# Kernel optimization log

Measured on AMD Instinct MI355X. Metric: run time of the kernel, lower is better.

Reference implementation:

```python
import jax, jax.numpy as jnp
import numpy as np

B, L, E, DK = 16, 2048, 1024, 128
MODE = "Decoder"


def setup_inputs() -> dict:
    key = jax.random.key(0)
    ks = jax.random.split(key, 6)
    x = jax.random.normal(ks[0], (B, L, E), dtype=jnp.float32)
    context = jax.random.normal(ks[1], (B, L, E), dtype=jnp.float32)
    batch_lengths = jax.random.randint(ks[2], (B,), 1, L + 1)  # valid lengths in [1, L]
    Wq = jax.random.normal(ks[3], (E, DK), dtype=jnp.float32) * 0.02
    Wk = jax.random.normal(ks[4], (E, DK), dtype=jnp.float32) * 0.02
    Wv = jax.random.normal(ks[5], (E, DK), dtype=jnp.float32) * 0.02
    return {"x": x, "context": context, "batch_lengths": batch_lengths,
            "Wq": Wq, "Wk": Wk, "Wv": Wv, "max_len": L}


def reference(x, context, batch_lengths, Wq, Wk, Wv, max_len):
    # x, context: [B, L, E]; batch_lengths: [B] ints; weights: [E, DK]
    Lq = x.shape[1]
    dk = Wq.shape[1]
    pos = jnp.arange(Lq)
    # outputMask: zero out padded time steps, broadcast over feature dim [B, L, 1]
    len_mask = (pos[None, :] < batch_lengths[:, None]).astype(x.dtype)[:, :, None]
    Q = (context @ Wq) * len_mask
    K = (context @ Wk) * len_mask
    V = (x @ Wv) * len_mask
    # energy: [B, Lq, Lk]
    energy = jnp.einsum("bqd,bkd->bqk", Q, K)
    # attnMask: -inf on padded key positions
    key_valid = pos[None, None, :] < batch_lengths[:, None, None]  # [B,1,Lk]
    if MODE == "Decoder":
        causal = pos[None, :, None] >= pos[None, None, :]  # j <= i
        key_valid = key_valid & causal
    energy = jnp.where(key_valid, energy, -jnp.inf)
    score = jax.nn.softmax(energy / jnp.sqrt(jnp.asarray(dk, x.dtype)), axis=-1)
    return jnp.einsum("bqk,bkd->bqd", score, V)
```

## Files before the change

kernel.cpp:

```cpp
#include <hip/hip_runtime.h>

#define DEV __device__ __forceinline__

typedef __attribute__((ext_vector_type(4))) float f32x4;
typedef __attribute__((ext_vector_type(4))) unsigned short u16x4;
typedef __attribute__((ext_vector_type(8))) __bf16 bf16x8;

constexpr int NB = 16, SL = 2048, EM = 1024, DKD = 128;

DEV unsigned short f2bf(float f) {
  unsigned int u = __float_as_uint(f);
  u += 0x7FFFu + ((u >> 16) & 1u);
  return (unsigned short)(u >> 16);
}

DEV f32x4 mfma16(bf16x8 a, bf16x8 b, f32x4 c) {
  return __builtin_amdgcn_mfma_f32_16x16x32_bf16(a, b, c, 0, 0, 0);
}

DEV void dma16(const void* g, void* l) {
  __builtin_amdgcn_global_load_lds(
      (const __attribute__((address_space(1))) unsigned int*)g,
      (__attribute__((address_space(3))) unsigned int*)l, 16, 0, 0);
}

DEV bf16x8 cvt8(f32x4 a, f32x4 b) {
  bf16x8 r;
  r[0] = (__bf16)a[0]; r[1] = (__bf16)a[1]; r[2] = (__bf16)a[2]; r[3] = (__bf16)a[3];
  r[4] = (__bf16)b[0]; r[5] = (__bf16)b[1]; r[6] = (__bf16)b[2]; r[7] = (__bf16)b[3];
  return r;
}

#define SBAR() __builtin_amdgcn_sched_barrier(0)

__global__ __launch_bounds__(256) void prep_w(
    const float* __restrict__ Wq, const float* __restrict__ Wk,
    const float* __restrict__ Wv, unsigned short* __restrict__ Wt)
{
  __shared__ unsigned short T[64 * 128];
  const int tid = threadIdx.x;
  const int m = blockIdx.x >> 4, kc = blockIdx.x & 15;
  const float* W = (m == 0) ? Wq : ((m == 1) ? Wk : Wv);
  #pragma unroll
  for (int it = 0; it < 8; ++it) {
    int idx = it * 256 + tid;
    int kk = idx >> 5, n4 = (idx & 31) * 4;
    f32x4 w4 = *(const f32x4*)(W + (size_t)(kc * 64 + kk) * DKD + n4);
    *(u16x4*)&T[kk * 128 + n4] =
        u16x4{ f2bf(w4[0]), f2bf(w4[1]), f2bf(w4[2]), f2bf(w4[3]) };
  }
  __syncthreads();
  #pragma unroll
  for (int it = 0; it < 4; ++it) {
    int idx = it * 256 + tid;
    int p = idx & 7, n = idx >> 3;
    int c = p ^ (n & 7);
    unsigned short v[8];
    #pragma unroll
    for (int e = 0; e < 8; ++e) v[e] = T[(c * 8 + e) * 128 + n];
    size_t t = ((size_t)(m * 16 + kc) * 128 + n) * 8 + p;
    *(u16x4*)(Wt + t * 8)     = u16x4{v[0], v[1], v[2], v[3]};
    *(u16x4*)(Wt + t * 8 + 4) = u16x4{v[4], v[5], v[6], v[7]};
  }
}

__global__ __launch_bounds__(256, 2) void proj_qk(
    const float* __restrict__ ctx, const unsigned short* __restrict__ Wt,
    const int* __restrict__ lens, unsigned short* __restrict__ Qo,
    unsigned short* __restrict__ Kz)
{
  __shared__ float Als[2][64 * 64];
  const int tid = threadIdx.x;
  const int wave = tid >> 6, lane = tid & 63;
  const int quad = lane >> 4, mm = lane & 15;
  const int rb = blockIdx.x * 64;
  const int len = lens[blockIdx.x >> 5];
  if ((rb & (SL - 1)) >= len) return;

  f32x4 acc[4][4];
  #pragma unroll
  for (int i = 0; i < 4; ++i)
    #pragma unroll
    for (int j = 0; j < 4; ++j) acc[i][j] = f32x4{0.f, 0.f, 0.f, 0.f};

  const float* asrc[4];
  #pragma unroll
  for (int i = 0; i < 4; ++i) {
    const int rl_ = wave * 16 + i * 4 + (lane >> 4);
    const int cc  = (lane & 8) | ((lane & 7) ^ (rl_ & 7));
    asrc[i] = ctx + (size_t)(rb + rl_) * EM + cc * 4;
  }
  int soff[2][2];
  #pragma unroll
  for (int ks = 0; ks < 2; ++ks) {
    soff[ks][0] = (ks * 8 + ((quad * 2)     ^ (mm & 7))) * 4;
    soff[ks][1] = (ks * 8 + ((quad * 2 + 1) ^ (mm & 7))) * 4;
  }
  const unsigned short* bbase[4][2];
  #pragma unroll
  for (int lo = 0; lo < 4; ++lo)
    #pragma unroll
    for (int ks = 0; ks < 2; ++ks) {
      const int nrow = (wave * 4 + lo) * 16 + mm;
      const int pp = (ks * 4 + quad) ^ (mm & 7);
      const int cs = nrow * 8 + pp;
      bbase[lo][ks] = Wt + ((size_t)(cs >> 10) * 16384 + (cs & 1023)) * 8;
    }

  #pragma unroll
  for (int i = 0; i < 4; ++i)
    dma16(asrc[i],      (char*)Als[0] + wave * 4096 + i * 1024);
  #pragma unroll
  for (int i = 0; i < 4; ++i)
    dma16(asrc[i] + 64, (char*)Als[1] + wave * 4096 + i * 1024);
  __asm__ volatile("s_waitcnt vmcnt(4)" ::: "memory");
  __builtin_amdgcn_s_barrier();

  #pragma unroll 1
  for (int kc = 0; kc < 16; ++kc) {
    SBAR();
    bf16x8 bfr[4][2];
    #pragma unroll
    for (int lo = 0; lo < 4; ++lo)
      #pragma unroll
      for (int ks = 0; ks < 2; ++ks)
        bfr[lo][ks] = *(const bf16x8*)(bbase[lo][ks] + (size_t)kc * 8192);
    bf16x8 af[4][2];
    #pragma unroll
    for (int rt = 0; rt < 4; ++rt) {
      const float* rbase = Als[kc & 1] + (rt * 16 + mm) * 64;
      #pragma unroll
      for (int ks = 0; ks < 2; ++ks) {
        f32x4 a0 = *(const f32x4*)(rbase + soff[ks][0]);
        f32x4 a1 = *(const f32x4*)(rbase + soff[ks][1]);
        af[rt][ks] = cvt8(a0, a1);
      }
    }
    __asm__ volatile("s_waitcnt lgkmcnt(0)" ::: "memory");
    SBAR();
    __builtin_amdgcn_s_barrier();
    {
      const int kn = (kc + 2 < 16) ? (kc + 2) : 15;
      #pragma unroll
      for (int i = 0; i < 4; ++i)
        dma16(asrc[i] + kn * 64, (char*)Als[kc & 1] + wave * 4096 + i * 1024);
    }
    #pragma unroll
    for (int lo = 0; lo < 4; ++lo)
      #pragma unroll
      for (int ks = 0; ks < 2; ++ks)
        #pragma unroll
        for (int rt = 0; rt < 4; ++rt)
          acc[rt][lo] = mfma16(af[rt][ks], bfr[lo][ks], acc[rt][lo]);
    __builtin_amdgcn_s_barrier();
  }
  __asm__ volatile("s_waitcnt vmcnt(0)" ::: "memory");

  const float SCALE = 1.4426950408889634f * 0.08838834764831845f;
  #pragma unroll
  for (int rt = 0; rt < 4; ++rt)
    #pragma unroll
    for (int lo = 0; lo < 4; ++lo) {
      const int ctg = wave * 4 + lo;
      #pragma unroll
      for (int reg = 0; reg < 4; ++reg) {
        const int row = rb + rt * 16 + quad * 4 + reg;
        const int j = row & (SL - 1);
        const float val = acc[rt][lo][reg];
        if (ctg < 8) {
          const int d = ctg * 16 + mm;
          Qo[(size_t)row * DKD + d] = f2bf(val * ((j < len) ? SCALE : 0.f));
        } else {
          const int d = (ctg - 8) * 16 + mm;
          Kz[(size_t)row * DKD + (((d >> 3) ^ (j & 15)) * 8) + (d & 7)] = f2bf(val);
        }
      }
    }
}

__global__ __launch_bounds__(256, 2) void proj_v(
    const float* __restrict__ x, const unsigned short* __restrict__ Wt,
    const int* __restrict__ lens, unsigned short* __restrict__ Vz)
{
  __shared__ float Als[2][64 * 64];
  const int tid = threadIdx.x;
  const int wave = tid >> 6, lane = tid & 63;
  const int quad = lane >> 4, mm = lane & 15;
  const int rb = blockIdx.x * 64;
  const int len = lens[blockIdx.x >> 5];
  if ((rb & (SL - 1)) >= len) return;

  f32x4 acc[4][2];
  #pragma unroll
  for (int i = 0; i < 4; ++i) { acc[i][0] = f32x4{0.f,0.f,0.f,0.f}; acc[i][1] = f32x4{0.f,0.f,0.f,0.f}; }

  const float* asrc[4];
  #pragma unroll
  for (int i = 0; i < 4; ++i) {
    const int rl_ = wave * 16 + i * 4 + (lane >> 4);
    const int cc  = (lane & 8) | ((lane & 7) ^ (rl_ & 7));
    asrc[i] = x + (size_t)(rb + rl_) * EM + cc * 4;
  }
  int soff[2][2];
  #pragma unroll
  for (int ks = 0; ks < 2; ++ks) {
    soff[ks][0] = (ks * 8 + ((quad * 2)     ^ (mm & 7))) * 4;
    soff[ks][1] = (ks * 8 + ((quad * 2 + 1) ^ (mm & 7))) * 4;
  }
  const unsigned short* bbase[2][2];
  #pragma unroll
  for (int lo = 0; lo < 2; ++lo)
    #pragma unroll
    for (int ks = 0; ks < 2; ++ks) {
      const int nrow = (wave * 2 + lo) * 16 + mm;
      const int pp = (ks * 4 + quad) ^ (mm & 7);
      const int cs = nrow * 8 + pp;
      bbase[lo][ks] = Wt + ((size_t)2 * 16384 + cs) * 8;
    }

  #pragma unroll
  for (int i = 0; i < 4; ++i)
    dma16(asrc[i],      (char*)Als[0] + wave * 4096 + i * 1024);
  #pragma unroll
  for (int i = 0; i < 4; ++i)
    dma16(asrc[i] + 64, (char*)Als[1] + wave * 4096 + i * 1024);
  __asm__ volatile("s_waitcnt vmcnt(4)" ::: "memory");
  __builtin_amdgcn_s_barrier();

  #pragma unroll 1
  for (int kc = 0; kc < 16; ++kc) {
    SBAR();
    bf16x8 bfr[2][2];
    #pragma unroll
    for (int lo = 0; lo < 2; ++lo)
      #pragma unroll
      for (int ks = 0; ks < 2; ++ks)
        bfr[lo][ks] = *(const bf16x8*)(bbase[lo][ks] + (size_t)kc * 8192);
    bf16x8 af[4][2];
    #pragma unroll
    for (int rt = 0; rt < 4; ++rt) {
      const float* rbase = Als[kc & 1] + (rt * 16 + mm) * 64;
      #pragma unroll
      for (int ks = 0; ks < 2; ++ks) {
        f32x4 a0 = *(const f32x4*)(rbase + soff[ks][0]);
        f32x4 a1 = *(const f32x4*)(rbase + soff[ks][1]);
        af[rt][ks] = cvt8(a0, a1);
      }
    }
    __asm__ volatile("s_waitcnt lgkmcnt(0)" ::: "memory");
    SBAR();
    __builtin_amdgcn_s_barrier();
    {
      const int kn = (kc + 2 < 16) ? (kc + 2) : 15;
      #pragma unroll
      for (int i = 0; i < 4; ++i)
        dma16(asrc[i] + kn * 64, (char*)Als[kc & 1] + wave * 4096 + i * 1024);
    }
    #pragma unroll
    for (int lo = 0; lo < 2; ++lo)
      #pragma unroll
      for (int ks = 0; ks < 2; ++ks)
        #pragma unroll
        for (int rt = 0; rt < 4; ++rt)
          acc[rt][lo] = mfma16(af[rt][ks], bfr[lo][ks], acc[rt][lo]);
    __builtin_amdgcn_s_barrier();
  }
  __asm__ volatile("s_waitcnt vmcnt(0)" ::: "memory");

  #pragma unroll
  for (int rt = 0; rt < 4; ++rt)
    #pragma unroll
    for (int lo = 0; lo < 2; ++lo) {
      const int d = (wave * 2 + lo) * 16 + mm;
      const int row0 = rb + rt * 16 + quad * 4;
      const int b = row0 >> 11, j0 = row0 & (SL - 1);
      u16x4 pk = u16x4{ f2bf(acc[rt][lo][0]), f2bf(acc[rt][lo][1]),
                        f2bf(acc[rt][lo][2]), f2bf(acc[rt][lo][3]) };
      size_t off = (size_t)b * DKD * SL + (size_t)d * SL + (j0 & ~63)
                 + ((((j0 >> 3) & 7) ^ (d & 7)) * 8) + (j0 & 7);
      *(u16x4*)(Vz + off) = pk;
    }
}

__global__ __launch_bounds__(256, 2) void attn(
    const unsigned short* __restrict__ Qw, const unsigned short* __restrict__ Kz,
    const unsigned short* __restrict__ Vz, const int* __restrict__ lens,
    float* __restrict__ out)
{
  __shared__ unsigned short Ks[2][64 * 128];
  __shared__ unsigned short Vs[2][128 * 64];
  __shared__ unsigned short Ps[4][16 * 72];
  __shared__ float mv[128];
  const int tid = threadIdx.x;
  const int wave = tid >> 6, lane = tid & 63;
  const int quad = lane >> 4, mm = lane & 15;
  const int b = blockIdx.y;
  const int qb = ((int)gridDim.x - 1 - (int)blockIdx.x) * 64;
  const int len = lens[b];

  if (qb >= len) {
    const int half = tid >> 7, d = tid & 127, d7 = d & 7;
    const unsigned short* vbase = Vz + (size_t)b * DKD * SL + (size_t)d * SL;
    float sum = 0.f;
    for (int j0 = half * 64; j0 < len; j0 += 128) {
      #pragma unroll
      for (int cc = 0; cc < 8; ++cc) {
        const int jstart = j0 + cc * 8;
        if (jstart >= len) break;
        const unsigned short* p = vbase + j0 + ((cc ^ d7) * 8);
        if (jstart + 8 <= len) {
          bf16x8 v = *(const bf16x8*)p;
          sum += (float)v[0] + (float)v[1] + (float)v[2] + (float)v[3]
               + (float)v[4] + (float)v[5] + (float)v[6] + (float)v[7];
        } else {
          for (int r = 0; r < 8; ++r)
            if (jstart + r < len) sum += (float)*(const __bf16*)(p + r);
        }
      }
    }
    if (half == 0) mv[d] = sum;
    __syncthreads();
    if (half == 1) mv[d] += sum;
    __syncthreads();
    const float val = mv[d] / (float)len;
    #pragma unroll 1
    for (int it = 0; it < 32; ++it) {
      const int row = qb + half + it * 2;
      out[((size_t)b * SL + row) * DKD + d] = val;
    }
    return;
  }

  const int kend = min(qb + 64, len);
  const int nblk = (kend + 63) >> 6;
  const int irow0 = qb + wave * 16 + quad * 4;

  bf16x8 aQ[4];
  {
    const unsigned short* qbase =
        Qw + (size_t)(b * SL + qb + wave * 16 + mm) * DKD + quad * 8;
    #pragma unroll
    for (int cc = 0; cc < 4; ++cc) aQ[cc] = *(const bf16x8*)(qbase + cc * 32);
  }
  float mr[4], lr[4];
  #pragma unroll
  for (int r = 0; r < 4; ++r) { mr[r] = -__builtin_inff(); lr[r] = 0.f; }
  f32x4 acc[8];
  #pragma unroll
  for (int i = 0; i < 8; ++i) acc[i] = f32x4{0.f,0.f,0.f,0.f};

  #pragma unroll
  for (int it = 0; it < 4; ++it) {
    int s = it * 256 + tid;
    dma16(Kz + (size_t)(b * SL) * DKD + (size_t)s * 8,
          (char*)Ks[0] + (it * 256 + wave * 64) * 16);
  }
  #pragma unroll
  for (int it = 0; it < 4; ++it) {
    int s = it * 256 + tid;
    int d = s >> 3, p = s & 7;
    dma16(Vz + (size_t)b * DKD * SL + (size_t)d * SL + p * 8,
          (char*)Vs[0] + (it * 256 + wave * 64) * 16);
  }

  #pragma unroll 1
  for (int blk = 0; blk < nblk; ++blk) {
    const int kb = blk * 64;
    __syncthreads();
    if (blk + 1 < nblk) {
      const int kb1 = kb + 64;
      const int nb = (blk + 1) & 1;
      #pragma unroll
      for (int it = 0; it < 4; ++it) {
        int s = it * 256 + tid;
        dma16(Kz + (size_t)(b * SL + kb1) * DKD + (size_t)s * 8,
              (char*)Ks[nb] + (it * 256 + wave * 64) * 16);
      }
      #pragma unroll
      for (int it = 0; it < 4; ++it) {
        int s = it * 256 + tid;
        int d = s >> 3, p = s & 7;
        dma16(Vz + (size_t)b * DKD * SL + (size_t)d * SL + kb1 + p * 8,
              (char*)Vs[nb] + (it * 256 + wave * 64) * 16);
      }
    }
    const unsigned short* kbuf = Ks[blk & 1];
    const unsigned short* vbuf = Vs[blk & 1];

    f32x4 s4[4];
    #pragma unroll
    for (int nt = 0; nt < 4; ++nt) {
      f32x4 c = f32x4{0.f,0.f,0.f,0.f};
      const int j = nt * 16 + mm;
      #pragma unroll
      for (int cc = 0; cc < 4; ++cc) {
        const int pp = (cc * 4 + quad) ^ mm;
        bf16x8 kf = *(const bf16x8*)(kbuf + j * 128 + pp * 8);
        c = mfma16(aQ[cc], kf, c);
      }
      s4[nt] = c;
    }

    float alpha[4];
    #pragma unroll
    for (int reg = 0; reg < 4; ++reg) {
      const int jl = min(irow0 + reg + 1, len);
      float v0 = (kb + mm      < jl) ? s4[0][reg] : -__builtin_inff();
      float v1 = (kb + 16 + mm < jl) ? s4[1][reg] : -__builtin_inff();
      float v2 = (kb + 32 + mm < jl) ? s4[2][reg] : -__builtin_inff();
      float v3 = (kb + 48 + mm < jl) ? s4[3][reg] : -__builtin_inff();
      float mx = fmaxf(fmaxf(v0, v1), fmaxf(v2, v3));
      #pragma unroll
      for (int xm = 1; xm < 16; xm <<= 1) mx = fmaxf(mx, __shfl_xor(mx, xm));
      const float mn = fmaxf(mr[reg], mx);
      alpha[reg] = __builtin_amdgcn_exp2f(mr[reg] - mn);
      const float p0 = __builtin_amdgcn_exp2f(v0 - mn);
      const float p1 = __builtin_amdgcn_exp2f(v1 - mn);
      const float p2 = __builtin_amdgcn_exp2f(v2 - mn);
      const float p3 = __builtin_amdgcn_exp2f(v3 - mn);
      float sm = (p0 + p1) + (p2 + p3);
      #pragma unroll
      for (int xm = 1; xm < 16; xm <<= 1) sm += __shfl_xor(sm, xm);
      lr[reg] = lr[reg] * alpha[reg] + sm;
      mr[reg] = mn;
      const int prow = quad * 4 + reg;
      Ps[wave][prow * 72 + mm]      = f2bf(p0);
      Ps[wave][prow * 72 + 16 + mm] = f2bf(p1);
      Ps[wave][prow * 72 + 32 + mm] = f2bf(p2);
      Ps[wave][prow * 72 + 48 + mm] = f2bf(p3);
    }
    #pragma unroll
    for (int nt = 0; nt < 8; ++nt) {
      f32x4 a = acc[nt];
      a[0] *= alpha[0]; a[1] *= alpha[1]; a[2] *= alpha[2]; a[3] *= alpha[3];
      acc[nt] = a;
    }
    __asm__ volatile("s_waitcnt lgkmcnt(0)" ::: "memory");
    bf16x8 aP[2];
    #pragma unroll
    for (int ks = 0; ks < 2; ++ks)
      aP[ks] = *(const bf16x8*)(&Ps[wave][mm * 72 + ks * 32 + quad * 8]);
    #pragma unroll
    for (int ks = 0; ks < 2; ++ks)
      #pragma unroll
      for (int nt = 0; nt < 8; ++nt) {
        const int pp = (ks * 4 + quad) ^ (mm & 7);
        bf16x8 vf = *(const bf16x8*)(vbuf + (nt * 16 + mm) * 64 + pp * 8);
        acc[nt] = mfma16(aP[ks], vf, acc[nt]);
      }
  }

  #pragma unroll
  for (int reg = 0; reg < 4; ++reg) {
    const float rl = 1.0f / lr[reg];
    const size_t base = ((size_t)b * SL + irow0 + reg) * DKD + mm;
    #pragma unroll
    for (int nt = 0; nt < 8; ++nt)
      out[base + nt * 16] = acc[nt][reg] * rl;
  }
}

extern "C" void kernel_launch(void* const* d_in, const int* in_sizes, int n_in,
                              void* d_out, int out_size, void* d_ws, size_t ws_size,
                              hipStream_t stream) {
  const float* x    = (const float*)d_in[0];
  const float* ctx  = (const float*)d_in[1];
  const int*   lens = (const int*)d_in[2];
  const float* Wq   = (const float*)d_in[3];
  const float* Wk   = (const float*)d_in[4];
  const float* Wv   = (const float*)d_in[5];
  float* out = (float*)d_out;

  const size_t QKV = (size_t)NB * SL * DKD * sizeof(unsigned short);
  const size_t WTSZ = (size_t)3 * 16 * 128 * 8 * 8 * sizeof(unsigned short);
  if (ws_size < 3 * QKV + WTSZ) return;
  unsigned short* Qws = (unsigned short*)d_ws;
  unsigned short* Kzs = (unsigned short*)((char*)d_ws + QKV);
  unsigned short* Vzs = (unsigned short*)((char*)d_ws + 2 * QKV);
  unsigned short* Wt  = (unsigned short*)((char*)d_ws + 3 * QKV);

  prep_w <<<dim3(48), 256, 0, stream>>>(Wq, Wk, Wv, Wt);
  proj_qk<<<dim3(NB * SL / 64), 256, 0, stream>>>(ctx, Wt, lens, Qws, Kzs);
  proj_v <<<dim3(NB * SL / 64), 256, 0, stream>>>(x, Wt, lens, Vzs);
  attn   <<<dim3(SL / 64, NB), 256, 0, stream>>>(Qws, Kzs, Vzs, lens, out);
}
```

Measured before the change: 353.4 us.

## Fuse padded-row V mean into proj_v; compute softmax denominator via MFMA

The per-batch V column sums needed for fully padded query rows are now accumulated inside proj_v with shuffles and atomics, instead of re-reading V from global memory in attn. The padded-row blocks then just broadcast the mean with vectorized stores. Separately, the softmax row-sum shuffle reduction is replaced by an extra MFMA of P against a ones vector, which removes cross-lane shuffles from the inner loop. The cost is global atomics, an extra zeroing step in prep_w, and a row sum taken from bf16-rounded probabilities.

```diff
diff --git a/kernel.cpp b/kernel.cpp
--- a/kernel.cpp
+++ b/kernel.cpp
@@ -35,10 +35,15 @@
 
 __global__ __launch_bounds__(256) void prep_w(
     const float* __restrict__ Wq, const float* __restrict__ Wk,
-    const float* __restrict__ Wv, unsigned short* __restrict__ Wt)
+    const float* __restrict__ Wv, unsigned short* __restrict__ Wt,
+    float* __restrict__ mvg)
 {
   __shared__ unsigned short T[64 * 128];
   const int tid = threadIdx.x;
+  if (blockIdx.x == 0) {
+    #pragma unroll
+    for (int i = 0; i < NB * DKD / 256; ++i) mvg[i * 256 + tid] = 0.f;
+  }
   const int m = blockIdx.x >> 4, kc = blockIdx.x & 15;
   const float* W = (m == 0) ? Wq : ((m == 1) ? Wk : Wv);
   #pragma unroll
@@ -180,14 +185,16 @@
 
 __global__ __launch_bounds__(256, 2) void proj_v(
     const float* __restrict__ x, const unsigned short* __restrict__ Wt,
-    const int* __restrict__ lens, unsigned short* __restrict__ Vz)
+    const int* __restrict__ lens, unsigned short* __restrict__ Vz,
+    float* __restrict__ mvg)
 {
   __shared__ float Als[2][64 * 64];
   const int tid = threadIdx.x;
   const int wave = tid >> 6, lane = tid & 63;
   const int quad = lane >> 4, mm = lane & 15;
   const int rb = blockIdx.x * 64;
-  const int len = lens[blockIdx.x >> 5];
+  const int bidx = blockIdx.x >> 5;
+  const int len = lens[bidx];
   if ((rb & (SL - 1)) >= len) return;
 
   f32x4 acc[4][2];
@@ -280,17 +287,33 @@
                  + ((((j0 >> 3) & 7) ^ (d & 7)) * 8) + (j0 & 7);
       *(u16x4*)(Vz + off) = pk;
     }
+
+  const int jb = rb & (SL - 1);
+  #pragma unroll
+  for (int lo = 0; lo < 2; ++lo) {
+    const int d = (wave * 2 + lo) * 16 + mm;
+    float part = 0.f;
+    #pragma unroll
+    for (int rt = 0; rt < 4; ++rt) {
+      const int jr = jb + rt * 16 + quad * 4;
+      #pragma unroll
+      for (int reg = 0; reg < 4; ++reg)
+        if (jr + reg < len) part += acc[rt][lo][reg];
+    }
+    part += __shfl_xor(part, 16);
+    part += __shfl_xor(part, 32);
+    if (quad == 0) atomicAdd(mvg + bidx * DKD + d, part);
+  }
 }
 
 __global__ __launch_bounds__(256, 2) void attn(
     const unsigned short* __restrict__ Qw, const unsigned short* __restrict__ Kz,
-    const unsigned short* __restrict__ Vz, const int* __restrict__ lens,
-    float* __restrict__ out)
+    const unsigned short* __restrict__ Vz, const float* __restrict__ mvg,
+    const int* __restrict__ lens, float* __restrict__ out)
 {
   __shared__ unsigned short Ks[2][64 * 128];
   __shared__ unsigned short Vs[2][128 * 64];
   __shared__ unsigned short Ps[4][16 * 72];
-  __shared__ float mv[128];
   const int tid = threadIdx.x;
   const int wave = tid >> 6, lane = tid & 63;
   const int quad = lane >> 4, mm = lane & 15;
@@ -299,34 +322,15 @@
   const int len = lens[b];
 
   if (qb >= len) {
-    const int half = tid >> 7, d = tid & 127, d7 = d & 7;
-    const unsigned short* vbase = Vz + (size_t)b * DKD * SL + (size_t)d * SL;
-    float sum = 0.f;
-    for (int j0 = half * 64; j0 < len; j0 += 128) {
-      #pragma unroll
-      for (int cc = 0; cc < 8; ++cc) {
-        const int jstart = j0 + cc * 8;
-        if (jstart >= len) break;
-        const unsigned short* p = vbase + j0 + ((cc ^ d7) * 8);
-        if (jstart + 8 <= len) {
-          bf16x8 v = *(const bf16x8*)p;
-          sum += (float)v[0] + (float)v[1] + (float)v[2] + (float)v[3]
-               + (float)v[4] + (float)v[5] + (float)v[6] + (float)v[7];
-        } else {
-          for (int r = 0; r < 8; ++r)
-            if (jstart + r < len) sum += (float)*(const __bf16*)(p + r);
-        }
-      }
-    }
-    if (half == 0) mv[d] = sum;
-    __syncthreads();
-    if (half == 1) mv[d] += sum;
-    __syncthreads();
-    const float val = mv[d] / (float)len;
-    #pragma unroll 1
-    for (int it = 0; it < 32; ++it) {
-      const int row = qb + half + it * 2;
-      out[((size_t)b * SL + row) * DKD + d] = val;
+    const int dd = (tid & 31) * 4;
+    const int r0 = tid >> 5;
+    const f32x4 m4 = *(const f32x4*)(mvg + b * DKD + dd);
+    const float inv = 1.0f / (float)len;
+    const f32x4 val = f32x4{ m4[0]*inv, m4[1]*inv, m4[2]*inv, m4[3]*inv };
+    #pragma unroll
+    for (int it = 0; it < 8; ++it) {
+      const int row = qb + it * 8 + r0;
+      *(f32x4*)(out + ((size_t)b * SL + row) * DKD + dd) = val;
     }
     return;
   }
@@ -342,12 +346,17 @@
     #pragma unroll
     for (int cc = 0; cc < 4; ++cc) aQ[cc] = *(const bf16x8*)(qbase + cc * 32);
   }
-  float mr[4], lr[4];
-  #pragma unroll
-  for (int r = 0; r < 4; ++r) { mr[r] = -__builtin_inff(); lr[r] = 0.f; }
+  bf16x8 onesb;
+  #pragma unroll
+  for (int i = 0; i < 8; ++i) onesb[i] = (__bf16)1.0f;
+
+  float mr[4];
+  #pragma unroll
+  for (int r = 0; r < 4; ++r) mr[r] = -__builtin_inff();
   f32x4 acc[8];
   #pragma unroll
   for (int i = 0; i < 8; ++i) acc[i] = f32x4{0.f,0.f,0.f,0.f};
+  f32x4 accl = f32x4{0.f,0.f,0.f,0.f};
 
   #pragma unroll
   for (int it = 0; it < 4; ++it) {
@@ -418,10 +427,6 @@
       const float p1 = __builtin_amdgcn_exp2f(v1 - mn);
       const float p2 = __builtin_amdgcn_exp2f(v2 - mn);
       const float p3 = __builtin_amdgcn_exp2f(v3 - mn);
-      float sm = (p0 + p1) + (p2 + p3);
-      #pragma unroll
-      for (int xm = 1; xm < 16; xm <<= 1) sm += __shfl_xor(sm, xm);
-      lr[reg] = lr[reg] * alpha[reg] + sm;
       mr[reg] = mn;
       const int prow = quad * 4 + reg;
       Ps[wave][prow * 72 + mm]      = f2bf(p0);
@@ -435,24 +440,28 @@
       a[0] *= alpha[0]; a[1] *= alpha[1]; a[2] *= alpha[2]; a[3] *= alpha[3];
       acc[nt] = a;
     }
+    accl[0] *= alpha[0]; accl[1] *= alpha[1];
+    accl[2] *= alpha[2]; accl[3] *= alpha[3];
     __asm__ volatile("s_waitcnt lgkmcnt(0)" ::: "memory");
     bf16x8 aP[2];
     #pragma unroll
     for (int ks = 0; ks < 2; ++ks)
       aP[ks] = *(const bf16x8*)(&Ps[wave][mm * 72 + ks * 32 + quad * 8]);
     #pragma unroll
-    for (int ks = 0; ks < 2; ++ks)
+    for (int ks = 0; ks < 2; ++ks) {
       #pragma unroll
       for (int nt = 0; nt < 8; ++nt) {
         const int pp = (ks * 4 + quad) ^ (mm & 7);
         bf16x8 vf = *(const bf16x8*)(vbuf + (nt * 16 + mm) * 64 + pp * 8);
         acc[nt] = mfma16(aP[ks], vf, acc[nt]);
       }
+      accl = mfma16(aP[ks], onesb, accl);
+    }
   }
 
   #pragma unroll
   for (int reg = 0; reg < 4; ++reg) {
-    const float rl = 1.0f / lr[reg];
+    const float rl = 1.0f / accl[reg];
     const size_t base = ((size_t)b * SL + irow0 + reg) * DKD + mm;
     #pragma unroll
     for (int nt = 0; nt < 8; ++nt)
@@ -473,14 +482,16 @@
 
   const size_t QKV = (size_t)NB * SL * DKD * sizeof(unsigned short);
   const size_t WTSZ = (size_t)3 * 16 * 128 * 8 * 8 * sizeof(unsigned short);
-  if (ws_size < 3 * QKV + WTSZ) return;
+  const size_t MVSZ = (size_t)NB * DKD * sizeof(float);
+  if (ws_size < 3 * QKV + WTSZ + MVSZ) return;
   unsigned short* Qws = (unsigned short*)d_ws;
   unsigned short* Kzs = (unsigned short*)((char*)d_ws + QKV);
   unsigned short* Vzs = (unsigned short*)((char*)d_ws + 2 * QKV);
   unsigned short* Wt  = (unsigned short*)((char*)d_ws + 3 * QKV);
-
-  prep_w <<<dim3(48), 256, 0, stream>>>(Wq, Wk, Wv, Wt);
+  float*          mvg = (float*)((char*)d_ws + 3 * QKV + WTSZ);
+
+  prep_w <<<dim3(48), 256, 0, stream>>>(Wq, Wk, Wv, Wt, mvg);
   proj_qk<<<dim3(NB * SL / 64), 256, 0, stream>>>(ctx, Wt, lens, Qws, Kzs);
-  proj_v <<<dim3(NB * SL / 64), 256, 0, stream>>>(x, Wt, lens, Vzs);
-  attn   <<<dim3(SL / 64, NB), 256, 0, stream>>>(Qws, Kzs, Vzs, lens, out);
-}
+  proj_v <<<dim3(NB * SL / 64), 256, 0, stream>>>(x, Wt, lens, Vzs, mvg);
+  attn   <<<dim3(SL / 64, NB), 256, 0, stream>>>(Qws, Kzs, Vzs, mvg, lens, out);
+}
```

New measurement: 346.8 us. Within noise of the previous version (-1.9%).
